# Kernel optimization log

Measured on AMD Instinct MI355X. Metric: run time of the kernel, lower is better.

Reference implementation:

```python
import jax, jax.numpy as jnp
import numpy as np

DEPTH = 100
HIDDEN = 1024
SHIFT = 25  # number of zeros prepended by the Shift module
LINEARITY = 0.97


def setup_inputs() -> dict:
    key = jax.random.key(0)
    ks = jax.random.split(key, 9)
    IN, OUT, B = 512, 512, 4096
    x = jax.random.normal(ks[0], (B, IN), dtype=jnp.float32)
    # torch Linear weight shape: [out, in]; xavier/kaiming init approximated by scaled normals
    fc1_w = jax.random.normal(ks[1], (HIDDEN, IN), dtype=jnp.float32) * (1.0 / np.sqrt(IN))
    fc1_b = jnp.zeros((HIDDEN,), dtype=jnp.float32)
    W1 = jax.random.normal(ks[2], (DEPTH, HIDDEN, HIDDEN), dtype=jnp.float32) * (1.0 / np.sqrt(HIDDEN))
    b1 = jnp.zeros((DEPTH, HIDDEN), dtype=jnp.float32)
    W2 = jax.random.normal(ks[3], (DEPTH, HIDDEN, HIDDEN), dtype=jnp.float32) * (np.sqrt(2.0) / np.sqrt(HIDDEN))
    b2 = jnp.zeros((DEPTH, HIDDEN), dtype=jnp.float32)
    fc2_w = jax.random.normal(ks[4], (OUT, HIDDEN), dtype=jnp.float32) * (1.0 / np.sqrt(HIDDEN))
    fc2_b = jnp.zeros((OUT,), dtype=jnp.float32)
    return {"x": x, "fc1_w": fc1_w, "fc1_b": fc1_b, "W1": W1, "b1": b1,
            "W2": W2, "b2": b2, "fc2_w": fc2_w, "fc2_b": fc2_b}


def _shift(x):
    # Shift: cat 25 zeros in front along last dim, then slice back to original width
    z = jnp.zeros_like(x[..., :SHIFT])
    return jnp.concatenate([z, x[..., :-SHIFT]], axis=-1)


def reference(x, fc1_w, fc1_b, W1, b1, W2, b2, fc2_w, fc2_b):
    x = x @ fc1_w.T + fc1_b  # [B, HIDDEN]

    def block(h, params):
        w1, bb1, w2, bb2 = params
        r = _shift(h)                       # shifted input is the residual
        a = jnp.maximum(r @ w1.T + bb1, 0)  # fc1 + clamp(min=0)
        y = a @ w2.T + bb2                  # fc2
        out = LINEARITY * r + (1.0 - LINEARITY) * y
        return out, None

    x, _ = jax.lax.scan(block, x, (W1, b1, W2, b2))
    return x @ fc2_w.T + fc2_b
```

## Files before the change

kernel.cpp:

```cpp
#include <hip/hip_runtime.h>
#include <cstdint>
#include <cstddef>

#define DEPTH 100
#define HID 1024
#define MROWS 4096
#define NSTEPS 202

typedef _Float16 half8 __attribute__((ext_vector_type(8)));
typedef float floatx4 __attribute__((ext_vector_type(4)));

__device__ __forceinline__ void gload_lds16_a(const void* g, void* l) {
    __builtin_amdgcn_global_load_lds((const __attribute__((address_space(1))) void*)g,
                                     (__attribute__((address_space(3))) void*)l, 16, 0, 1);
}
__device__ __forceinline__ void gload_lds16_w(const void* g, void* l) {
    __builtin_amdgcn_global_load_lds((const __attribute__((address_space(1))) void*)g,
                                     (__attribute__((address_space(3))) void*)l, 16, 0, 2);
}

__global__ __launch_bounds__(512, 1)
void resnet_persist(const _Float16* __restrict__ xh, const _Float16* __restrict__ fc1h,
                    const float* __restrict__ fc1_b,
                    const _Float16* __restrict__ W1h, const float* __restrict__ b1,
                    const _Float16* __restrict__ W2h, const float* __restrict__ b2,
                    const _Float16* __restrict__ fc2h, const float* __restrict__ fc2_b,
                    float* __restrict__ hsA, float* __restrict__ hsB,
                    _Float16* __restrict__ rb, _Float16* __restrict__ ab,
                    float* __restrict__ outp, unsigned* __restrict__ ctr)
{
    __shared__ _Float16 As[3][128 * 64];
    __shared__ _Float16 Bs[3][128 * 64];
    __shared__ float    Hs[128 * 128];

    const int tid = threadIdx.x;
    const int l   = tid & 63;
    const int w   = tid >> 6;
    const int wm  = w >> 2;
    const int wn  = w & 3;

    const int lr = l >> 3;
    const int lj = l & 7;
    const int sw = (l & 7) << 4;

    unsigned xcd_s;
    asm volatile("s_getreg_b32 %0, hwreg(HW_REG_XCC_ID)" : "=s"(xcd_s));
    unsigned* shm = (unsigned*)Hs;
    if (tid == 0) {
        const unsigned x = xcd_s & 7u;
        const unsigned r = __hip_atomic_fetch_add(&ctr[x], 1u, __ATOMIC_RELAXED, __HIP_MEMORY_SCOPE_AGENT);
        __hip_atomic_fetch_add(&ctr[8], 1u, __ATOMIC_RELEASE, __HIP_MEMORY_SCOPE_AGENT);
        while (__hip_atomic_load(&ctr[8], __ATOMIC_RELAXED, __HIP_MEMORY_SCOPE_AGENT) < 256u)
            __builtin_amdgcn_s_sleep(2);
        __builtin_amdgcn_fence(__ATOMIC_ACQUIRE, "agent");
        unsigned ok = 1u;
        for (int i2 = 0; i2 < 8; ++i2)
            ok &= (__hip_atomic_load(&ctr[i2], __ATOMIC_RELAXED, __HIP_MEMORY_SCOPE_AGENT) == 32u) ? 1u : 0u;
        shm[0] = r; shm[1] = ok; shm[2] = x;
    }
    __syncthreads();
    const unsigned rank  = shm[0];
    const unsigned okf   = shm[1];
    const unsigned myxcd = shm[2];
    __syncthreads();

    const float C1 = 0.97f;
    const float C2 = (float)(1.0 - 0.97);

    for (int s = 0; s < NSTEPS; ++s) {
        if (s > 0) {
            asm volatile("s_waitcnt vmcnt(0) lgkmcnt(0)" ::: "memory");
            __syncthreads();
            if (okf) {
                if (tid == 0) {
                    unsigned* slot = &ctr[16 + (s - 1) * 8 + (int)myxcd];
                    __hip_atomic_fetch_add(slot, 1u, __ATOMIC_RELAXED, __HIP_MEMORY_SCOPE_AGENT);
                    while (__hip_atomic_load(slot, __ATOMIC_RELAXED, __HIP_MEMORY_SCOPE_AGENT) < 32u)
                        __builtin_amdgcn_s_sleep(2);
                }
                __syncthreads();
                __builtin_amdgcn_sched_barrier(0);
            } else {
                if (tid == 0) {
                    unsigned* slot = &ctr[2048 + (s - 1)];
                    __hip_atomic_fetch_add(slot, 1u, __ATOMIC_RELEASE, __HIP_MEMORY_SCOPE_AGENT);
                    while (__hip_atomic_load(slot, __ATOMIC_RELAXED, __HIP_MEMORY_SCOPE_AGENT) < 256u)
                        __builtin_amdgcn_s_sleep(4);
                }
                __syncthreads();
                __builtin_amdgcn_fence(__ATOMIC_ACQUIRE, "agent");
            }
        }

        const _Float16* A; const _Float16* B; const float* bias;
        const float* hsrd = nullptr; float* hswr = nullptr;
        int K, mode, rshift = 0;
        if (s == 0) {
            A = xh; B = fc1h; bias = fc1_b; K = 512; mode = 0;
            hswr = hsA; rshift = 25;
        } else if (s == NSTEPS - 1) {
            A = rb; B = fc2h; bias = fc2_b; K = HID; mode = 3;
        } else {
            const int d = (s - 1) >> 1;
            if (s & 1) {
                A = rb; B = W1h + (size_t)d * HID * HID; bias = b1 + d * HID;
                K = HID; mode = 1;
            } else {
                A = ab; B = W2h + (size_t)d * HID * HID; bias = b2 + d * HID;
                K = HID; mode = 2;
                hsrd = (d & 1) ? hsB : hsA;
                hswr = (d & 1) ? hsA : hsB;
                rshift = (d == DEPTH - 1) ? 0 : 25;
            }
        }

        int bm, bn; bool active = true;
        if (okf) {
            if (mode == 3) {
                if (rank < 16u) { bm = (int)myxcd * 4 + (int)(rank >> 2); bn = (int)(rank & 3u); }
                else { active = false; bm = 0; bn = 0; }
            } else {
                bm = (int)myxcd * 4 + (int)(rank >> 3); bn = (int)(rank & 7u);
            }
        } else {
            const int b0  = blockIdx.x;
            const int bid = (b0 & 7) * 32 + (b0 >> 3);
            if (mode == 3) {
                if (bid < 128) { bm = bid >> 2; bn = bid & 3; }
                else { active = false; bm = 0; bn = 0; }
            } else {
                bn = bid & 7; bm = bid >> 3;
            }
        }
        if (!active) continue;

        const int colb = bn * 128 + wn * 32 + (l & 15);
        const int rowb = bm * 128 + wm * 64 + ((l >> 4) << 2);

        if (mode == 2) {
            #pragma unroll
            for (int q = 0; q < 8; ++q) {
                const int chunk = w * 8 + q;
                const int row   = chunk * 2 + (l >> 5);
                const int c16   = l & 31;
                gload_lds16_a((const void*)(hsrd + (size_t)(bm * 128 + row) * HID + bn * 128 + c16 * 4),
                              (void*)((char*)Hs + chunk * 1024));
            }
        }

        floatx4 acc[4][2];
        const floatx4 zero = {0.f, 0.f, 0.f, 0.f};
        #pragma unroll
        for (int i = 0; i < 4; ++i)
            #pragma unroll
            for (int j = 0; j < 2; ++j) acc[i][j] = zero;

        auto stage = [&](int buf, int kt) {
            #pragma unroll
            for (int q = 0; q < 2; ++q) {
                const int c   = w * 2 + q;
                const int row = c * 8 + lr;
                const int jch = lj ^ (row & 7);
                gload_lds16_a((const void*)(A + (size_t)(bm * 128 + row) * K + kt * 64 + jch * 8),
                              (void*)((char*)As[buf] + c * 1024));
            }
            #pragma unroll
            for (int q = 0; q < 2; ++q) {
                const int c   = w * 2 + q;
                const int row = c * 8 + lr;
                const int jch = lj ^ (row & 7);
                gload_lds16_w((const void*)(B + (size_t)(bn * 128 + row) * K + kt * 64 + jch * 8),
                              (void*)((char*)Bs[buf] + c * 1024));
            }
        };

        auto compute = [&](int buf) {
            #pragma unroll
            for (int kk = 0; kk < 2; ++kk) {
                half8 af[4], bf[2];
                #pragma unroll
                for (int fi = 0; fi < 4; ++fi) {
                    const int off = ((wm * 64 + fi * 16 + (l & 15)) * 128 + kk * 64 + ((l >> 4) << 4)) ^ sw;
                    af[fi] = *(const half8*)((const char*)As[buf] + off);
                }
                #pragma unroll
                for (int fj = 0; fj < 2; ++fj) {
                    const int off = ((wn * 32 + fj * 16 + (l & 15)) * 128 + kk * 64 + ((l >> 4) << 4)) ^ sw;
                    bf[fj] = *(const half8*)((const char*)Bs[buf] + off);
                }
                __builtin_amdgcn_s_setprio(1);
                #pragma unroll
                for (int fi = 0; fi < 4; ++fi)
                    #pragma unroll
                    for (int fj = 0; fj < 2; ++fj)
                        acc[fi][fj] = __builtin_amdgcn_mfma_f32_16x16x32_f16(af[fi], bf[fj], acc[fi][fj], 0, 0, 0);
                __builtin_amdgcn_s_setprio(0);
            }
        };

        const int nkt = K >> 6;
        stage(0, 0);
        stage(1, 1);
        int cur = 0;
        for (int kt = 0; kt < nkt; ++kt) {
            if (kt + 2 < nkt) {
                int n2 = cur + 2; if (n2 >= 3) n2 -= 3;
                stage(n2, kt + 2);
            }
            const int rem   = nkt - 1 - kt;
            const int ahead = rem < 2 ? rem : 2;
            if (ahead == 2)      asm volatile("s_waitcnt vmcnt(8)" ::: "memory");
            else if (ahead == 1) asm volatile("s_waitcnt vmcnt(4)" ::: "memory");
            else                 asm volatile("s_waitcnt vmcnt(0)" ::: "memory");
            __builtin_amdgcn_s_barrier();
            __builtin_amdgcn_sched_barrier(0);
            compute(cur);
            __builtin_amdgcn_s_barrier();
            cur = (cur + 1 == 3) ? 0 : cur + 1;
        }

        __builtin_amdgcn_sched_barrier(0);
        #pragma unroll
        for (int fi = 0; fi < 4; ++fi) {
            #pragma unroll
            for (int fj = 0; fj < 2; ++fj) {
                const int j = colb + fj * 16;
                const float bj = bias[j];
                #pragma unroll
                for (int v = 0; v < 4; ++v) {
                    const int i = rowb + fi * 16 + v;
                    const float val = acc[fi][fj][v] + bj;
                    if (mode == 1) {
                        ab[(size_t)i * HID + j] = (_Float16)fmaxf(val, 0.f);
                    } else if (mode == 3) {
                        outp[(size_t)i * 512 + j] = val;
                    } else {
                        float hv;
                        if (mode == 2) {
                            const int rowl = wm * 64 + fi * 16 + ((l >> 4) << 2) + v;
                            const int coll = wn * 32 + fj * 16 + (l & 15);
                            const float r = Hs[rowl * 128 + (coll ^ (((rowl >> 2) & 1) << 4))];
                            hv = C1 * r + C2 * val;
                        } else {
                            hv = val;
                        }
                        if (rshift == 0) {
                            rb[(size_t)i * HID + j] = (_Float16)hv;
                        } else {
                            const int jd = j + 25;
                            if (jd < HID) {
                                rb[(size_t)i * HID + jd] = (_Float16)hv;
                                hswr[(size_t)i * HID + (jd & ~127) + ((jd & 127) ^ (((i >> 2) & 1) << 4))] = hv;
                            }
                            if (j < 25) {
                                rb[(size_t)i * HID + j] = (_Float16)0.f;
                                hswr[(size_t)i * HID + (j ^ (((i >> 2) & 1) << 4))] = 0.f;
                            }
                        }
                    }
                }
            }
        }
    }
}

__global__ void cvt_kernel(const float* __restrict__ in, _Float16* __restrict__ out, long n8)
{
    const long stride = (long)gridDim.x * 256;
    for (long idx = (long)blockIdx.x * 256 + threadIdx.x; idx < n8; idx += stride) {
        const floatx4 f0 = ((const floatx4*)in)[idx * 2];
        const floatx4 f1 = ((const floatx4*)in)[idx * 2 + 1];
        half8 h;
        #pragma unroll
        for (int i = 0; i < 4; ++i) {
            h[i]     = (_Float16)f0[i];
            h[4 + i] = (_Float16)f1[i];
        }
        ((half8*)out)[idx] = h;
    }
}

__global__ void zero_ctr(unsigned* __restrict__ ctr, int n)
{
    const int i = blockIdx.x * 256 + threadIdx.x;
    if (i < n) ctr[i] = 0u;
}

static inline void launch_cvt(const float* in, _Float16* out, long n, hipStream_t s)
{
    const long n8 = n / 8;
    int blocks = (int)((n8 + 255) / 256);
    if (blocks > 2048) blocks = 2048;
    cvt_kernel<<<dim3(blocks), dim3(256), 0, s>>>(in, out, n8);
}

extern "C" void kernel_launch(void* const* d_in, const int* in_sizes, int n_in,
                              void* d_out, int out_size, void* d_ws, size_t ws_size,
                              hipStream_t stream)
{
    (void)in_sizes; (void)n_in; (void)out_size; (void)ws_size;
    const float* x     = (const float*)d_in[0];
    const float* fc1_w = (const float*)d_in[1];
    const float* fc1_b = (const float*)d_in[2];
    const float* W1    = (const float*)d_in[3];
    const float* b1    = (const float*)d_in[4];
    const float* W2    = (const float*)d_in[5];
    const float* b2    = (const float*)d_in[6];
    const float* fc2_w = (const float*)d_in[7];
    const float* fc2_b = (const float*)d_in[8];
    float* out = (float*)d_out;

    char* ws = (char*)d_ws;
    _Float16* xh   = (_Float16*)(ws);
    _Float16* rb   = (_Float16*)(ws + (4ull   << 20));
    _Float16* ab   = (_Float16*)(ws + (12ull  << 20));
    float*    hsA  = (float*)   (ws + (20ull  << 20));
    float*    hsB  = (float*)   (ws + (36ull  << 20));
    _Float16* fc1h = (_Float16*)(ws + (52ull  << 20));
    _Float16* fc2h = (_Float16*)(ws + (53ull  << 20));
    _Float16* W1h  = (_Float16*)(ws + (54ull  << 20));
    _Float16* W2h  = (_Float16*)(ws + (254ull << 20));
    unsigned* ctr  = (unsigned*)(ws + (460ull << 20));

    launch_cvt(x, xh, (long)MROWS * 512, stream);
    launch_cvt(fc1_w, fc1h, (long)HID * 512, stream);
    launch_cvt(W1,    W1h,  (long)DEPTH * HID * HID, stream);
    launch_cvt(W2,    W2h,  (long)DEPTH * HID * HID, stream);
    launch_cvt(fc2_w, fc2h, (long)512 * HID, stream);
    zero_ctr<<<dim3(16), dim3(256), 0, stream>>>(ctr, 4096);

    resnet_persist<<<dim3(256), dim3(512), 0, stream>>>(
        xh, fc1h, fc1_b, W1h, b1, W2h, b2, fc2h, fc2_b,
        hsA, hsB, rb, ab, out, ctr);
}
```

Measured before the change: 5.689 ms.

## Split K-loop into half-steps interleaving A/B prefetch and pad sync counters

Restructures the GEMM main loop so each 64-wide K tile is processed in two halves. The A-tile prefetch is issued during the first half and the B-tile prefetch during the second, with barriers and a single vmcnt wait per tile instead of one wait before each compute. Separately, the inter-block sync counters are padded to 128-byte spacing to avoid false sharing between atomics, which requires zeroing a larger counter region. The goal is better overlap of global-to-LDS loads with MFMA work and less atomic contention, at the cost of extra barriers per tile.

```diff
diff --git a/kernel.cpp b/kernel.cpp
--- a/kernel.cpp
+++ b/kernel.cpp
@@ -48,14 +48,14 @@
     unsigned* shm = (unsigned*)Hs;
     if (tid == 0) {
         const unsigned x = xcd_s & 7u;
-        const unsigned r = __hip_atomic_fetch_add(&ctr[x], 1u, __ATOMIC_RELAXED, __HIP_MEMORY_SCOPE_AGENT);
-        __hip_atomic_fetch_add(&ctr[8], 1u, __ATOMIC_RELEASE, __HIP_MEMORY_SCOPE_AGENT);
-        while (__hip_atomic_load(&ctr[8], __ATOMIC_RELAXED, __HIP_MEMORY_SCOPE_AGENT) < 256u)
+        const unsigned r = __hip_atomic_fetch_add(&ctr[x * 32], 1u, __ATOMIC_RELAXED, __HIP_MEMORY_SCOPE_AGENT);
+        __hip_atomic_fetch_add(&ctr[8 * 32], 1u, __ATOMIC_RELEASE, __HIP_MEMORY_SCOPE_AGENT);
+        while (__hip_atomic_load(&ctr[8 * 32], __ATOMIC_RELAXED, __HIP_MEMORY_SCOPE_AGENT) < 256u)
             __builtin_amdgcn_s_sleep(2);
         __builtin_amdgcn_fence(__ATOMIC_ACQUIRE, "agent");
         unsigned ok = 1u;
         for (int i2 = 0; i2 < 8; ++i2)
-            ok &= (__hip_atomic_load(&ctr[i2], __ATOMIC_RELAXED, __HIP_MEMORY_SCOPE_AGENT) == 32u) ? 1u : 0u;
+            ok &= (__hip_atomic_load(&ctr[i2 * 32], __ATOMIC_RELAXED, __HIP_MEMORY_SCOPE_AGENT) == 32u) ? 1u : 0u;
         shm[0] = r; shm[1] = ok; shm[2] = x;
     }
     __syncthreads();
@@ -73,7 +73,7 @@
             __syncthreads();
             if (okf) {
                 if (tid == 0) {
-                    unsigned* slot = &ctr[16 + (s - 1) * 8 + (int)myxcd];
+                    unsigned* slot = &ctr[(1024 + ((s - 1) * 8 + (int)myxcd)) * 32];
                     __hip_atomic_fetch_add(slot, 1u, __ATOMIC_RELAXED, __HIP_MEMORY_SCOPE_AGENT);
                     while (__hip_atomic_load(slot, __ATOMIC_RELAXED, __HIP_MEMORY_SCOPE_AGENT) < 32u)
                         __builtin_amdgcn_s_sleep(2);
@@ -82,7 +82,7 @@
                 __builtin_amdgcn_sched_barrier(0);
             } else {
                 if (tid == 0) {
-                    unsigned* slot = &ctr[2048 + (s - 1)];
+                    unsigned* slot = &ctr[(1024 + 2048 + (s - 1)) * 32];
                     __hip_atomic_fetch_add(slot, 1u, __ATOMIC_RELEASE, __HIP_MEMORY_SCOPE_AGENT);
                     while (__hip_atomic_load(slot, __ATOMIC_RELAXED, __HIP_MEMORY_SCOPE_AGENT) < 256u)
                         __builtin_amdgcn_s_sleep(4);
@@ -155,7 +155,7 @@
             #pragma unroll
             for (int j = 0; j < 2; ++j) acc[i][j] = zero;
 
-        auto stage = [&](int buf, int kt) {
+        auto stageA = [&](int buf, int kt) {
             #pragma unroll
             for (int q = 0; q < 2; ++q) {
                 const int c   = w * 2 + q;
@@ -164,6 +164,8 @@
                 gload_lds16_a((const void*)(A + (size_t)(bm * 128 + row) * K + kt * 64 + jch * 8),
                               (void*)((char*)As[buf] + c * 1024));
             }
+        };
+        auto stageB = [&](int buf, int kt) {
             #pragma unroll
             for (int q = 0; q < 2; ++q) {
                 const int c   = w * 2 + q;
@@ -174,20 +176,33 @@
             }
         };
 
-        auto compute = [&](int buf) {
-            #pragma unroll
-            for (int kk = 0; kk < 2; ++kk) {
+        const int nkt = K >> 6;
+        stageA(0, 0); stageB(0, 0);
+        stageA(1, 1); stageB(1, 1);
+        asm volatile("s_waitcnt vmcnt(4)" ::: "memory");
+        __builtin_amdgcn_s_barrier();
+
+        int cur = 0;
+        for (int kt = 0; kt < nkt; ++kt) {
+            int n2 = cur + 2; if (n2 >= 3) n2 -= 3;
+            const bool pre = (kt + 2 < nkt);
+
+            {
                 half8 af[4], bf[2];
                 #pragma unroll
                 for (int fi = 0; fi < 4; ++fi) {
-                    const int off = ((wm * 64 + fi * 16 + (l & 15)) * 128 + kk * 64 + ((l >> 4) << 4)) ^ sw;
-                    af[fi] = *(const half8*)((const char*)As[buf] + off);
+                    const int off = ((wm * 64 + fi * 16 + (l & 15)) * 128 + ((l >> 4) << 4)) ^ sw;
+                    af[fi] = *(const half8*)((const char*)As[cur] + off);
                 }
                 #pragma unroll
                 for (int fj = 0; fj < 2; ++fj) {
-                    const int off = ((wn * 32 + fj * 16 + (l & 15)) * 128 + kk * 64 + ((l >> 4) << 4)) ^ sw;
-                    bf[fj] = *(const half8*)((const char*)Bs[buf] + off);
-                }
+                    const int off = ((wn * 32 + fj * 16 + (l & 15)) * 128 + ((l >> 4) << 4)) ^ sw;
+                    bf[fj] = *(const half8*)((const char*)Bs[cur] + off);
+                }
+                if (pre) stageA(n2, kt + 2);
+                __builtin_amdgcn_s_barrier();
+                asm volatile("s_waitcnt lgkmcnt(0)" ::: "memory");
+                __builtin_amdgcn_sched_barrier(0);
                 __builtin_amdgcn_s_setprio(1);
                 #pragma unroll
                 for (int fi = 0; fi < 4; ++fi)
@@ -195,27 +210,37 @@
                     for (int fj = 0; fj < 2; ++fj)
                         acc[fi][fj] = __builtin_amdgcn_mfma_f32_16x16x32_f16(af[fi], bf[fj], acc[fi][fj], 0, 0, 0);
                 __builtin_amdgcn_s_setprio(0);
-            }
-        };
-
-        const int nkt = K >> 6;
-        stage(0, 0);
-        stage(1, 1);
-        int cur = 0;
-        for (int kt = 0; kt < nkt; ++kt) {
-            if (kt + 2 < nkt) {
-                int n2 = cur + 2; if (n2 >= 3) n2 -= 3;
-                stage(n2, kt + 2);
-            }
-            const int rem   = nkt - 1 - kt;
-            const int ahead = rem < 2 ? rem : 2;
-            if (ahead == 2)      asm volatile("s_waitcnt vmcnt(8)" ::: "memory");
-            else if (ahead == 1) asm volatile("s_waitcnt vmcnt(4)" ::: "memory");
-            else                 asm volatile("s_waitcnt vmcnt(0)" ::: "memory");
-            __builtin_amdgcn_s_barrier();
-            __builtin_amdgcn_sched_barrier(0);
-            compute(cur);
-            __builtin_amdgcn_s_barrier();
+                __builtin_amdgcn_s_barrier();
+            }
+            {
+                half8 af[4], bf[2];
+                #pragma unroll
+                for (int fi = 0; fi < 4; ++fi) {
+                    const int off = ((wm * 64 + fi * 16 + (l & 15)) * 128 + 64 + ((l >> 4) << 4)) ^ sw;
+                    af[fi] = *(const half8*)((const char*)As[cur] + off);
+                }
+                #pragma unroll
+                for (int fj = 0; fj < 2; ++fj) {
+                    const int off = ((wn * 32 + fj * 16 + (l & 15)) * 128 + 64 + ((l >> 4) << 4)) ^ sw;
+                    bf[fj] = *(const half8*)((const char*)Bs[cur] + off);
+                }
+                if (pre) stageB(n2, kt + 2);
+                __builtin_amdgcn_s_barrier();
+                asm volatile("s_waitcnt lgkmcnt(0)" ::: "memory");
+                __builtin_amdgcn_sched_barrier(0);
+                __builtin_amdgcn_s_setprio(1);
+                #pragma unroll
+                for (int fi = 0; fi < 4; ++fi)
+                    #pragma unroll
+                    for (int fj = 0; fj < 2; ++fj)
+                        acc[fi][fj] = __builtin_amdgcn_mfma_f32_16x16x32_f16(af[fi], bf[fj], acc[fi][fj], 0, 0, 0);
+                __builtin_amdgcn_s_setprio(0);
+                if (kt < nkt - 1) {
+                    if (pre) asm volatile("s_waitcnt vmcnt(4)" ::: "memory");
+                    else     asm volatile("s_waitcnt vmcnt(0)" ::: "memory");
+                }
+                __builtin_amdgcn_s_barrier();
+            }
             cur = (cur + 1 == 3) ? 0 : cur + 1;
         }
 
@@ -327,7 +352,7 @@
     launch_cvt(W1,    W1h,  (long)DEPTH * HID * HID, stream);
     launch_cvt(W2,    W2h,  (long)DEPTH * HID * HID, stream);
     launch_cvt(fc2_w, fc2h, (long)512 * HID, stream);
-    zero_ctr<<<dim3(16), dim3(256), 0, stream>>>(ctr, 4096);
+    zero_ctr<<<dim3(512), dim3(256), 0, stream>>>(ctr, 131072);
 
     resnet_persist<<<dim3(256), dim3(512), 0, stream>>>(
         xh, fc1h, fc1_b, W1h, b1, W2h, b2, fc2h, fc2_b,
```

After: 5.549 ms. -2.5%, faster.

## Split persistent GEMM into 512 blocks of 128x64 tiles with padded counters

Applied to the files above, without the earlier changes.

Relaunches the persistent kernel as 512 blocks of 256 threads, each owning a 128x64 output tile instead of 128x128. The goal is to use two workgroups per CU and make better use of the machine. The residual is now read straight from global memory in the epilogue instead of being prefetched into LDS, so the swizzled hs layout is dropped. Barrier counters are spaced 32 words apart to avoid false sharing. The costs are twice as many A-tile reloads, barriers that must now gather 512 arrivals instead of 256, and uncoalesced scalar residual loads on the epilogue's critical path.

```diff
diff --git a/kernel.cpp b/kernel.cpp
--- a/kernel.cpp
+++ b/kernel.cpp
@@ -18,8 +18,11 @@
     __builtin_amdgcn_global_load_lds((const __attribute__((address_space(1))) void*)g,
                                      (__attribute__((address_space(3))) void*)l, 16, 0, 2);
 }
-
-__global__ __launch_bounds__(512, 1)
+__device__ __forceinline__ float ld_sc0_f32(const float* p) {
+    return __hip_atomic_load(p, __ATOMIC_RELAXED, __HIP_MEMORY_SCOPE_AGENT);
+}
+
+__global__ __launch_bounds__(256, 1)
 void resnet_persist(const _Float16* __restrict__ xh, const _Float16* __restrict__ fc1h,
                     const float* __restrict__ fc1_b,
                     const _Float16* __restrict__ W1h, const float* __restrict__ b1,
@@ -30,14 +33,13 @@
                     float* __restrict__ outp, unsigned* __restrict__ ctr)
 {
     __shared__ _Float16 As[3][128 * 64];
-    __shared__ _Float16 Bs[3][128 * 64];
-    __shared__ float    Hs[128 * 128];
+    __shared__ _Float16 Bs[3][64 * 64];
 
     const int tid = threadIdx.x;
     const int l   = tid & 63;
     const int w   = tid >> 6;
-    const int wm  = w >> 2;
-    const int wn  = w & 3;
+    const int wm  = w >> 1;
+    const int wn  = w & 1;
 
     const int lr = l >> 3;
     const int lj = l & 7;
@@ -45,17 +47,17 @@
 
     unsigned xcd_s;
     asm volatile("s_getreg_b32 %0, hwreg(HW_REG_XCC_ID)" : "=s"(xcd_s));
-    unsigned* shm = (unsigned*)Hs;
+    __shared__ unsigned shm[4];
     if (tid == 0) {
         const unsigned x = xcd_s & 7u;
-        const unsigned r = __hip_atomic_fetch_add(&ctr[x], 1u, __ATOMIC_RELAXED, __HIP_MEMORY_SCOPE_AGENT);
-        __hip_atomic_fetch_add(&ctr[8], 1u, __ATOMIC_RELEASE, __HIP_MEMORY_SCOPE_AGENT);
-        while (__hip_atomic_load(&ctr[8], __ATOMIC_RELAXED, __HIP_MEMORY_SCOPE_AGENT) < 256u)
+        const unsigned r = __hip_atomic_fetch_add(&ctr[x * 32], 1u, __ATOMIC_RELAXED, __HIP_MEMORY_SCOPE_AGENT);
+        __hip_atomic_fetch_add(&ctr[8 * 32], 1u, __ATOMIC_RELEASE, __HIP_MEMORY_SCOPE_AGENT);
+        while (__hip_atomic_load(&ctr[8 * 32], __ATOMIC_RELAXED, __HIP_MEMORY_SCOPE_AGENT) < 512u)
             __builtin_amdgcn_s_sleep(2);
         __builtin_amdgcn_fence(__ATOMIC_ACQUIRE, "agent");
         unsigned ok = 1u;
         for (int i2 = 0; i2 < 8; ++i2)
-            ok &= (__hip_atomic_load(&ctr[i2], __ATOMIC_RELAXED, __HIP_MEMORY_SCOPE_AGENT) == 32u) ? 1u : 0u;
+            ok &= (__hip_atomic_load(&ctr[i2 * 32], __ATOMIC_RELAXED, __HIP_MEMORY_SCOPE_AGENT) == 64u) ? 1u : 0u;
         shm[0] = r; shm[1] = ok; shm[2] = x;
     }
     __syncthreads();
@@ -73,18 +75,18 @@
             __syncthreads();
             if (okf) {
                 if (tid == 0) {
-                    unsigned* slot = &ctr[16 + (s - 1) * 8 + (int)myxcd];
+                    unsigned* slot = &ctr[(1024 + ((s - 1) * 8 + (int)myxcd)) * 32];
                     __hip_atomic_fetch_add(slot, 1u, __ATOMIC_RELAXED, __HIP_MEMORY_SCOPE_AGENT);
-                    while (__hip_atomic_load(slot, __ATOMIC_RELAXED, __HIP_MEMORY_SCOPE_AGENT) < 32u)
+                    while (__hip_atomic_load(slot, __ATOMIC_RELAXED, __HIP_MEMORY_SCOPE_AGENT) < 64u)
                         __builtin_amdgcn_s_sleep(2);
                 }
                 __syncthreads();
                 __builtin_amdgcn_sched_barrier(0);
             } else {
                 if (tid == 0) {
-                    unsigned* slot = &ctr[2048 + (s - 1)];
+                    unsigned* slot = &ctr[(1024 + 2048 + (s - 1)) * 32];
                     __hip_atomic_fetch_add(slot, 1u, __ATOMIC_RELEASE, __HIP_MEMORY_SCOPE_AGENT);
-                    while (__hip_atomic_load(slot, __ATOMIC_RELAXED, __HIP_MEMORY_SCOPE_AGENT) < 256u)
+                    while (__hip_atomic_load(slot, __ATOMIC_RELAXED, __HIP_MEMORY_SCOPE_AGENT) < 512u)
                         __builtin_amdgcn_s_sleep(4);
                 }
                 __syncthreads();
@@ -117,36 +119,22 @@
         int bm, bn; bool active = true;
         if (okf) {
             if (mode == 3) {
-                if (rank < 16u) { bm = (int)myxcd * 4 + (int)(rank >> 2); bn = (int)(rank & 3u); }
+                if ((rank & 15u) < 8u) { bm = (int)myxcd * 4 + (int)(rank >> 4); bn = (int)(rank & 7u); }
                 else { active = false; bm = 0; bn = 0; }
             } else {
-                bm = (int)myxcd * 4 + (int)(rank >> 3); bn = (int)(rank & 7u);
+                bm = (int)myxcd * 4 + (int)(rank >> 4); bn = (int)(rank & 15u);
             }
         } else {
             const int b0  = blockIdx.x;
-            const int bid = (b0 & 7) * 32 + (b0 >> 3);
+            const int bid = (b0 & 7) * 64 + (b0 >> 3);
             if (mode == 3) {
-                if (bid < 128) { bm = bid >> 2; bn = bid & 3; }
+                if ((bid & 15) < 8) { bm = bid >> 4; bn = bid & 7; }
                 else { active = false; bm = 0; bn = 0; }
             } else {
-                bn = bid & 7; bm = bid >> 3;
+                bm = bid >> 4; bn = bid & 15;
             }
         }
         if (!active) continue;
-
-        const int colb = bn * 128 + wn * 32 + (l & 15);
-        const int rowb = bm * 128 + wm * 64 + ((l >> 4) << 2);
-
-        if (mode == 2) {
-            #pragma unroll
-            for (int q = 0; q < 8; ++q) {
-                const int chunk = w * 8 + q;
-                const int row   = chunk * 2 + (l >> 5);
-                const int c16   = l & 31;
-                gload_lds16_a((const void*)(hsrd + (size_t)(bm * 128 + row) * HID + bn * 128 + c16 * 4),
-                              (void*)((char*)Hs + chunk * 1024));
-            }
-        }
 
         floatx4 acc[4][2];
         const floatx4 zero = {0.f, 0.f, 0.f, 0.f};
@@ -157,19 +145,19 @@
 
         auto stage = [&](int buf, int kt) {
             #pragma unroll
+            for (int q = 0; q < 4; ++q) {
+                const int c   = w * 4 + q;
+                const int row = c * 8 + lr;
+                const int jch = lj ^ (row & 7);
+                gload_lds16_a((const void*)(A + (size_t)(bm * 128 + row) * K + kt * 64 + jch * 8),
+                              (void*)((char*)As[buf] + c * 1024));
+            }
+            #pragma unroll
             for (int q = 0; q < 2; ++q) {
                 const int c   = w * 2 + q;
                 const int row = c * 8 + lr;
                 const int jch = lj ^ (row & 7);
-                gload_lds16_a((const void*)(A + (size_t)(bm * 128 + row) * K + kt * 64 + jch * 8),
-                              (void*)((char*)As[buf] + c * 1024));
-            }
-            #pragma unroll
-            for (int q = 0; q < 2; ++q) {
-                const int c   = w * 2 + q;
-                const int row = c * 8 + lr;
-                const int jch = lj ^ (row & 7);
-                gload_lds16_w((const void*)(B + (size_t)(bn * 128 + row) * K + kt * 64 + jch * 8),
+                gload_lds16_w((const void*)(B + (size_t)(bn * 64 + row) * K + kt * 64 + jch * 8),
                               (void*)((char*)Bs[buf] + c * 1024));
             }
         };
@@ -209,9 +197,9 @@
             }
             const int rem   = nkt - 1 - kt;
             const int ahead = rem < 2 ? rem : 2;
-            if (ahead == 2)      asm volatile("s_waitcnt vmcnt(8)" ::: "memory");
-            else if (ahead == 1) asm volatile("s_waitcnt vmcnt(4)" ::: "memory");
-            else                 asm volatile("s_waitcnt vmcnt(0)" ::: "memory");
+            if (ahead == 2)      asm volatile("s_waitcnt vmcnt(12)" ::: "memory");
+            else if (ahead == 1) asm volatile("s_waitcnt vmcnt(6)"  ::: "memory");
+            else                 asm volatile("s_waitcnt vmcnt(0)"  ::: "memory");
             __builtin_amdgcn_s_barrier();
             __builtin_amdgcn_sched_barrier(0);
             compute(cur);
@@ -219,7 +207,8 @@
             cur = (cur + 1 == 3) ? 0 : cur + 1;
         }
 
-        __builtin_amdgcn_sched_barrier(0);
+        const int colb = bn * 64 + wn * 32 + (l & 15);
+        const int rowb = bm * 128 + wm * 64 + ((l >> 4) << 2);
         #pragma unroll
         for (int fi = 0; fi < 4; ++fi) {
             #pragma unroll
@@ -237,9 +226,7 @@
                     } else {
                         float hv;
                         if (mode == 2) {
-                            const int rowl = wm * 64 + fi * 16 + ((l >> 4) << 2) + v;
-                            const int coll = wn * 32 + fj * 16 + (l & 15);
-                            const float r = Hs[rowl * 128 + (coll ^ (((rowl >> 2) & 1) << 4))];
+                            const float r = ld_sc0_f32(hsrd + (size_t)i * HID + j);
                             hv = C1 * r + C2 * val;
                         } else {
                             hv = val;
@@ -249,12 +236,12 @@
                         } else {
                             const int jd = j + 25;
                             if (jd < HID) {
-                                rb[(size_t)i * HID + jd] = (_Float16)hv;
-                                hswr[(size_t)i * HID + (jd & ~127) + ((jd & 127) ^ (((i >> 2) & 1) << 4))] = hv;
+                                rb[(size_t)i * HID + jd]   = (_Float16)hv;
+                                hswr[(size_t)i * HID + jd] = hv;
                             }
                             if (j < 25) {
-                                rb[(size_t)i * HID + j] = (_Float16)0.f;
-                                hswr[(size_t)i * HID + (j ^ (((i >> 2) & 1) << 4))] = 0.f;
+                                rb[(size_t)i * HID + j]   = (_Float16)0.f;
+                                hswr[(size_t)i * HID + j] = 0.f;
                             }
                         }
                     }
@@ -327,9 +314,9 @@
     launch_cvt(W1,    W1h,  (long)DEPTH * HID * HID, stream);
     launch_cvt(W2,    W2h,  (long)DEPTH * HID * HID, stream);
     launch_cvt(fc2_w, fc2h, (long)512 * HID, stream);
-    zero_ctr<<<dim3(16), dim3(256), 0, stream>>>(ctr, 4096);
-
-    resnet_persist<<<dim3(256), dim3(512), 0, stream>>>(
+    zero_ctr<<<dim3(512), dim3(256), 0, stream>>>(ctr, 131072);
+
+    resnet_persist<<<dim3(512), dim3(256), 0, stream>>>(
         xh, fc1h, fc1_b, W1h, b1, W2h, b2, fc2h, fc2_b,
         hsA, hsB, rb, ab, out, ctr);
 }
```

Result: slower. 6.182 ms (+8.7%).

## Keep fp32 residual tile in LDS and exchange only 25-column shift halo

Applied to the files above, without the earlier changes.

The full fp32 residual array in global memory (hsA/hsB) is replaced by keeping each block's output tile in LDS across steps. Only the 25 boundary columns that the shift moves into the neighbouring column tile are exchanged through a small global staging buffer, read back with agent-scope loads. Sync counters are also padded to separate cache lines, and the B loads are issued before the A loads. This cuts global traffic per residual step, but it relies on each block keeping the same tile every step and adds an extra __syncthreads in the epilogue.

```diff
diff --git a/kernel.cpp b/kernel.cpp
--- a/kernel.cpp
+++ b/kernel.cpp
@@ -17,6 +17,9 @@
 __device__ __forceinline__ void gload_lds16_w(const void* g, void* l) {
     __builtin_amdgcn_global_load_lds((const __attribute__((address_space(1))) void*)g,
                                      (__attribute__((address_space(3))) void*)l, 16, 0, 2);
+}
+__device__ __forceinline__ float ld_sc0_f32(const float* p) {
+    return __hip_atomic_load(p, __ATOMIC_RELAXED, __HIP_MEMORY_SCOPE_AGENT);
 }
 
 __global__ __launch_bounds__(512, 1)
@@ -25,13 +28,13 @@
                     const _Float16* __restrict__ W1h, const float* __restrict__ b1,
                     const _Float16* __restrict__ W2h, const float* __restrict__ b2,
                     const _Float16* __restrict__ fc2h, const float* __restrict__ fc2_b,
-                    float* __restrict__ hsA, float* __restrict__ hsB,
-                    _Float16* __restrict__ rb, _Float16* __restrict__ ab,
-                    float* __restrict__ outp, unsigned* __restrict__ ctr)
+                    float* __restrict__ Sst, _Float16* __restrict__ rb,
+                    _Float16* __restrict__ ab, float* __restrict__ outp,
+                    unsigned* __restrict__ ctr)
 {
     __shared__ _Float16 As[3][128 * 64];
     __shared__ _Float16 Bs[3][128 * 64];
-    __shared__ float    Hs[128 * 128];
+    __shared__ float    Ht[128 * 128];
 
     const int tid = threadIdx.x;
     const int l   = tid & 63;
@@ -45,17 +48,17 @@
 
     unsigned xcd_s;
     asm volatile("s_getreg_b32 %0, hwreg(HW_REG_XCC_ID)" : "=s"(xcd_s));
-    unsigned* shm = (unsigned*)Hs;
+    unsigned* shm = (unsigned*)Ht;
     if (tid == 0) {
         const unsigned x = xcd_s & 7u;
-        const unsigned r = __hip_atomic_fetch_add(&ctr[x], 1u, __ATOMIC_RELAXED, __HIP_MEMORY_SCOPE_AGENT);
-        __hip_atomic_fetch_add(&ctr[8], 1u, __ATOMIC_RELEASE, __HIP_MEMORY_SCOPE_AGENT);
-        while (__hip_atomic_load(&ctr[8], __ATOMIC_RELAXED, __HIP_MEMORY_SCOPE_AGENT) < 256u)
+        const unsigned r = __hip_atomic_fetch_add(&ctr[x * 32], 1u, __ATOMIC_RELAXED, __HIP_MEMORY_SCOPE_AGENT);
+        __hip_atomic_fetch_add(&ctr[8 * 32], 1u, __ATOMIC_RELEASE, __HIP_MEMORY_SCOPE_AGENT);
+        while (__hip_atomic_load(&ctr[8 * 32], __ATOMIC_RELAXED, __HIP_MEMORY_SCOPE_AGENT) < 256u)
             __builtin_amdgcn_s_sleep(2);
         __builtin_amdgcn_fence(__ATOMIC_ACQUIRE, "agent");
         unsigned ok = 1u;
         for (int i2 = 0; i2 < 8; ++i2)
-            ok &= (__hip_atomic_load(&ctr[i2], __ATOMIC_RELAXED, __HIP_MEMORY_SCOPE_AGENT) == 32u) ? 1u : 0u;
+            ok &= (__hip_atomic_load(&ctr[i2 * 32], __ATOMIC_RELAXED, __HIP_MEMORY_SCOPE_AGENT) == 32u) ? 1u : 0u;
         shm[0] = r; shm[1] = ok; shm[2] = x;
     }
     __syncthreads();
@@ -66,6 +69,7 @@
 
     const float C1 = 0.97f;
     const float C2 = (float)(1.0 - 0.97);
+    const size_t SBUF = (size_t)32 * 9 * 128 * 25;
 
     for (int s = 0; s < NSTEPS; ++s) {
         if (s > 0) {
@@ -73,7 +77,7 @@
             __syncthreads();
             if (okf) {
                 if (tid == 0) {
-                    unsigned* slot = &ctr[16 + (s - 1) * 8 + (int)myxcd];
+                    unsigned* slot = &ctr[(1024 + ((s - 1) * 8 + (int)myxcd)) * 32];
                     __hip_atomic_fetch_add(slot, 1u, __ATOMIC_RELAXED, __HIP_MEMORY_SCOPE_AGENT);
                     while (__hip_atomic_load(slot, __ATOMIC_RELAXED, __HIP_MEMORY_SCOPE_AGENT) < 32u)
                         __builtin_amdgcn_s_sleep(2);
@@ -82,7 +86,7 @@
                 __builtin_amdgcn_sched_barrier(0);
             } else {
                 if (tid == 0) {
-                    unsigned* slot = &ctr[2048 + (s - 1)];
+                    unsigned* slot = &ctr[(1024 + 2048 + (s - 1)) * 32];
                     __hip_atomic_fetch_add(slot, 1u, __ATOMIC_RELEASE, __HIP_MEMORY_SCOPE_AGENT);
                     while (__hip_atomic_load(slot, __ATOMIC_RELAXED, __HIP_MEMORY_SCOPE_AGENT) < 256u)
                         __builtin_amdgcn_s_sleep(4);
@@ -93,11 +97,10 @@
         }
 
         const _Float16* A; const _Float16* B; const float* bias;
-        const float* hsrd = nullptr; float* hswr = nullptr;
-        int K, mode, rshift = 0;
+        int K, mode, rshift = 0, rbuf = 0, wbuf = 0;
         if (s == 0) {
             A = xh; B = fc1h; bias = fc1_b; K = 512; mode = 0;
-            hswr = hsA; rshift = 25;
+            rshift = 25; wbuf = 0;
         } else if (s == NSTEPS - 1) {
             A = rb; B = fc2h; bias = fc2_b; K = HID; mode = 3;
         } else {
@@ -108,8 +111,7 @@
             } else {
                 A = ab; B = W2h + (size_t)d * HID * HID; bias = b2 + d * HID;
                 K = HID; mode = 2;
-                hsrd = (d & 1) ? hsB : hsA;
-                hswr = (d & 1) ? hsA : hsB;
+                rbuf = d & 1; wbuf = 1 - rbuf;
                 rshift = (d == DEPTH - 1) ? 0 : 25;
             }
         }
@@ -129,24 +131,10 @@
                 if (bid < 128) { bm = bid >> 2; bn = bid & 3; }
                 else { active = false; bm = 0; bn = 0; }
             } else {
-                bn = bid & 7; bm = bid >> 3;
+                bm = bid >> 3; bn = bid & 7;
             }
         }
         if (!active) continue;
-
-        const int colb = bn * 128 + wn * 32 + (l & 15);
-        const int rowb = bm * 128 + wm * 64 + ((l >> 4) << 2);
-
-        if (mode == 2) {
-            #pragma unroll
-            for (int q = 0; q < 8; ++q) {
-                const int chunk = w * 8 + q;
-                const int row   = chunk * 2 + (l >> 5);
-                const int c16   = l & 31;
-                gload_lds16_a((const void*)(hsrd + (size_t)(bm * 128 + row) * HID + bn * 128 + c16 * 4),
-                              (void*)((char*)Hs + chunk * 1024));
-            }
-        }
 
         floatx4 acc[4][2];
         const floatx4 zero = {0.f, 0.f, 0.f, 0.f};
@@ -156,6 +144,14 @@
             for (int j = 0; j < 2; ++j) acc[i][j] = zero;
 
         auto stage = [&](int buf, int kt) {
+            #pragma unroll
+            for (int q = 0; q < 2; ++q) {
+                const int c   = w * 2 + q;
+                const int row = c * 8 + lr;
+                const int jch = lj ^ (row & 7);
+                gload_lds16_w((const void*)(B + (size_t)(bn * 128 + row) * K + kt * 64 + jch * 8),
+                              (void*)((char*)Bs[buf] + c * 1024));
+            }
             #pragma unroll
             for (int q = 0; q < 2; ++q) {
                 const int c   = w * 2 + q;
@@ -163,14 +159,6 @@
                 const int jch = lj ^ (row & 7);
                 gload_lds16_a((const void*)(A + (size_t)(bm * 128 + row) * K + kt * 64 + jch * 8),
                               (void*)((char*)As[buf] + c * 1024));
-            }
-            #pragma unroll
-            for (int q = 0; q < 2; ++q) {
-                const int c   = w * 2 + q;
-                const int row = c * 8 + lr;
-                const int jch = lj ^ (row & 7);
-                gload_lds16_w((const void*)(B + (size_t)(bn * 128 + row) * K + kt * 64 + jch * 8),
-                              (void*)((char*)Bs[buf] + c * 1024));
             }
         };
 
@@ -219,47 +207,77 @@
             cur = (cur + 1 == 3) ? 0 : cur + 1;
         }
 
-        __builtin_amdgcn_sched_barrier(0);
-        #pragma unroll
-        for (int fi = 0; fi < 4; ++fi) {
-            #pragma unroll
-            for (int fj = 0; fj < 2; ++fj) {
-                const int j = colb + fj * 16;
-                const float bj = bias[j];
-                #pragma unroll
-                for (int v = 0; v < 4; ++v) {
-                    const int i = rowb + fi * 16 + v;
-                    const float val = acc[fi][fj][v] + bj;
-                    if (mode == 1) {
-                        ab[(size_t)i * HID + j] = (_Float16)fmaxf(val, 0.f);
-                    } else if (mode == 3) {
-                        outp[(size_t)i * 512 + j] = val;
-                    } else {
-                        float hv;
-                        if (mode == 2) {
-                            const int rowl = wm * 64 + fi * 16 + ((l >> 4) << 2) + v;
-                            const int coll = wn * 32 + fj * 16 + (l & 15);
-                            const float r = Hs[rowl * 128 + (coll ^ (((rowl >> 2) & 1) << 4))];
-                            hv = C1 * r + C2 * val;
-                        } else {
-                            hv = val;
+        const int colb = bn * 128 + wn * 32 + (l & 15);
+        const int rowb = bm * 128 + wm * 64 + ((l >> 4) << 2);
+        const int jl0  = wn * 32 + (l & 15);
+        const int il0  = wm * 64 + ((l >> 4) << 2);
+
+        if (mode == 1) {
+            #pragma unroll
+            for (int fi = 0; fi < 4; ++fi)
+                #pragma unroll
+                for (int fj = 0; fj < 2; ++fj) {
+                    const int j = colb + fj * 16;
+                    const float bj = bias[j];
+                    #pragma unroll
+                    for (int v = 0; v < 4; ++v)
+                        ab[(size_t)(rowb + fi * 16 + v) * HID + j] = (_Float16)fmaxf(acc[fi][fj][v] + bj, 0.f);
+                }
+        } else if (mode == 3) {
+            #pragma unroll
+            for (int fi = 0; fi < 4; ++fi)
+                #pragma unroll
+                for (int fj = 0; fj < 2; ++fj) {
+                    const int j = colb + fj * 16;
+                    const float bj = bias[j];
+                    #pragma unroll
+                    for (int v = 0; v < 4; ++v)
+                        outp[(size_t)(rowb + fi * 16 + v) * 512 + j] = acc[fi][fj][v] + bj;
+                }
+        } else {
+            float rv[4][2][4];
+            if (mode == 2) {
+                const float* Srd = Sst + (size_t)rbuf * SBUF + ((size_t)(bm * 9 + bn) * 128) * 25;
+                #pragma unroll
+                for (int fi = 0; fi < 4; ++fi)
+                    #pragma unroll
+                    for (int fj = 0; fj < 2; ++fj) {
+                        const int jl = jl0 + fj * 16;
+                        #pragma unroll
+                        for (int v = 0; v < 4; ++v) {
+                            const int il = il0 + fi * 16 + v;
+                            if (jl >= 25)      rv[fi][fj][v] = Ht[il * 128 + (jl - 25)];
+                            else if (bn > 0)   rv[fi][fj][v] = ld_sc0_f32(Srd + il * 25 + jl);
+                            else               rv[fi][fj][v] = 0.f;
                         }
+                    }
+                __syncthreads();
+            }
+            float* Swr = Sst + (size_t)wbuf * SBUF + ((size_t)(bm * 9 + bn + 1) * 128) * 25;
+            #pragma unroll
+            for (int fi = 0; fi < 4; ++fi)
+                #pragma unroll
+                for (int fj = 0; fj < 2; ++fj) {
+                    const int j  = colb + fj * 16;
+                    const int jl = jl0 + fj * 16;
+                    const float bj = bias[j];
+                    #pragma unroll
+                    for (int v = 0; v < 4; ++v) {
+                        const int i  = rowb + fi * 16 + v;
+                        const int il = il0 + fi * 16 + v;
+                        const float val = acc[fi][fj][v] + bj;
+                        const float hv = (mode == 2) ? (C1 * rv[fi][fj][v] + C2 * val) : val;
+                        Ht[il * 128 + jl] = hv;
                         if (rshift == 0) {
                             rb[(size_t)i * HID + j] = (_Float16)hv;
                         } else {
                             const int jd = j + 25;
-                            if (jd < HID) {
-                                rb[(size_t)i * HID + jd] = (_Float16)hv;
-                                hswr[(size_t)i * HID + (jd & ~127) + ((jd & 127) ^ (((i >> 2) & 1) << 4))] = hv;
-                            }
-                            if (j < 25) {
-                                rb[(size_t)i * HID + j] = (_Float16)0.f;
-                                hswr[(size_t)i * HID + (j ^ (((i >> 2) & 1) << 4))] = 0.f;
-                            }
+                            if (jd < HID) rb[(size_t)i * HID + jd] = (_Float16)hv;
+                            if (j < 25)   rb[(size_t)i * HID + j]  = (_Float16)0.f;
+                            if (jl >= 103) Swr[il * 25 + (jl - 103)] = hv;
                         }
                     }
                 }
-            }
         }
     }
 }
@@ -314,22 +332,21 @@
     _Float16* xh   = (_Float16*)(ws);
     _Float16* rb   = (_Float16*)(ws + (4ull   << 20));
     _Float16* ab   = (_Float16*)(ws + (12ull  << 20));
-    float*    hsA  = (float*)   (ws + (20ull  << 20));
-    float*    hsB  = (float*)   (ws + (36ull  << 20));
     _Float16* fc1h = (_Float16*)(ws + (52ull  << 20));
     _Float16* fc2h = (_Float16*)(ws + (53ull  << 20));
     _Float16* W1h  = (_Float16*)(ws + (54ull  << 20));
     _Float16* W2h  = (_Float16*)(ws + (254ull << 20));
     unsigned* ctr  = (unsigned*)(ws + (460ull << 20));
+    float*    Sst  = (float*)   (ws + (468ull << 20));
 
     launch_cvt(x, xh, (long)MROWS * 512, stream);
     launch_cvt(fc1_w, fc1h, (long)HID * 512, stream);
     launch_cvt(W1,    W1h,  (long)DEPTH * HID * HID, stream);
     launch_cvt(W2,    W2h,  (long)DEPTH * HID * HID, stream);
     launch_cvt(fc2_w, fc2h, (long)512 * HID, stream);
-    zero_ctr<<<dim3(16), dim3(256), 0, stream>>>(ctr, 4096);
+    zero_ctr<<<dim3(512), dim3(256), 0, stream>>>(ctr, 131072);
 
     resnet_persist<<<dim3(256), dim3(512), 0, stream>>>(
         xh, fc1h, fc1_b, W1h, b1, W2h, b2, fc2h, fc2_b,
-        hsA, hsB, rb, ab, out, ctr);
-}
+        Sst, rb, ab, out, ctr);
+}
```

New measurement: 5.037 ms. 11.5% less time.
